# Kernel optimization log

Measured on AMD Instinct MI355X. Metric: run time of the kernel, lower is better.

## Reference

```python
import jax, jax.numpy as jnp
import numpy as np


def setup_inputs() -> dict:
    key = jax.random.key(0)
    ks = jax.random.split(key, 8)
    T, B, O, H, A = 512, 256, 720, 128, 2
    s = lambda k, shp, sc: (jax.random.normal(k, shp, jnp.float32) * sc)
    return {
        "x": jax.random.normal(ks[0], (T, B, O), jnp.float32),
        "h0": jnp.zeros((B, H), jnp.float32),
        "c0": jnp.zeros((B, H), jnp.float32),
        "Wx": s(ks[1], (O, 4 * H), 1.0 / np.sqrt(O)),
        "Wh": s(ks[2], (H, 4 * H), 1.0 / np.sqrt(H)),
        "b": jnp.zeros((4 * H,), jnp.float32),
        "Wa1": s(ks[3], (H, H), np.sqrt(2.0 / H)),
        "ba1": jnp.zeros((H,), jnp.float32),
        "Wa2": s(ks[4], (H, A), 0.01),
        "ba2": jnp.zeros((A,), jnp.float32),
        "log_std": jnp.zeros((A,), jnp.float32),
        "Wc1": s(ks[5], (H, H), np.sqrt(2.0 / H)),
        "bc1": jnp.zeros((H,), jnp.float32),
        "Wc2": s(ks[6], (H, 1), 0.01),
        "bc2": jnp.zeros((1,), jnp.float32),
    }


def _lstm(x, h0, c0, Wx, Wh, b):
    # Precompute input projections for all timesteps: [T, B, 4H]
    xW = jnp.einsum('tbo,og->tbg', x, Wx) + b

    def step(carry, xw_t):
        h, c = carry
        gates = xw_t + h @ Wh  # [B, 4H]
        i, f, g, o = jnp.split(gates, 4, axis=-1)
        c = jax.nn.sigmoid(f) * c + jax.nn.sigmoid(i) * jnp.tanh(g)
        h = jax.nn.sigmoid(o) * jnp.tanh(c)
        return (h, c), h

    (hT, cT), _ = jax.lax.scan(step, (h0, c0), xW)
    return hT, cT


def reference(x, h0, c0, Wx, Wh, b, Wa1, ba1, Wa2, ba2, log_std,
              Wc1, bc1, Wc2, bc2):
    hT, cT = _lstm(x, h0, c0, Wx, Wh, b)
    feat = hT  # outputs[-1] == last hidden state (unidirectional)
    actor_mean = jnp.tanh(feat @ Wa1 + ba1) @ Wa2 + ba2  # [B, A]
    std = jnp.exp(log_std)  # [A]
    value = (jnp.tanh(feat @ Wc1 + bc1) @ Wc2 + bc2).squeeze(-1)  # [B]
    return actor_mean, std, value, hT, cT
```

## Files before the change

kernel.cpp:

```cpp
#include <hip/hip_runtime.h>
#include <hip/hip_bf16.h>

typedef unsigned int   u32;
typedef unsigned short u16;
typedef _Float16       f16;
typedef __attribute__((ext_vector_type(2))) _Float16 f16x2;
typedef __attribute__((ext_vector_type(8))) _Float16 f16x8;
typedef __attribute__((ext_vector_type(4))) float    f32x4;
typedef __attribute__((ext_vector_type(4))) u32      u32x4;

#define T_STEPS 512
#define BATCH   256
#define O_IN    720
#define KPAD    736
#define HID     128
#define G4      512
#define OUT_STD 512
#define OUT_VAL 514
#define OUT_HT  770
#define OUT_CT  33538

static const unsigned long long XW_OFF  = 0ull;
static const unsigned long long WXT_OFF = 134217728ull;

__device__ inline float exp2raw(float x){
  float r; asm("v_exp_f32 %0, %1" : "=v"(r) : "v"(x)); return r;
}
__device__ inline float rcpraw(float x){
  float r; asm("v_rcp_f32 %0, %1" : "=v"(r) : "v"(x)); return r;
}
__device__ inline float tanhfast(float x){
  return fmaf(2.f, rcpraw(1.0f + exp2raw(-2.88539008f * x)), -1.f);
}

__device__ inline float dot2f(u32 a, u32 b, float c){
  float d;
  asm("v_dot2_f32_f16 %0, %1, %2, %3" : "=v"(d) : "v"(a), "v"(b), "v"(c));
  return d;
}

#define HH_STRIDE 144
#define H_BYTES   (2*HH_STRIDE)
#define HW_OFF(j) (((j)>>6)*HH_STRIDE + ((j)&63)*2)

__global__ void k_pack_wxt(const float* __restrict__ Wx, u16* __restrict__ wxt){
  const int n = blockIdx.x;
  for (int k = threadIdx.x; k < KPAD; k += 256){
    float v = (k < O_IN) ? Wx[(size_t)k * G4 + n] : 0.f;
    wxt[(size_t)n * KPAD + k] = __builtin_bit_cast(u16, (f16)v);
  }
}

__global__ __launch_bounds__(256, 2) void k_gemm(const float* __restrict__ x,
                                                 const u16* __restrict__ wxt,
                                                 u16* __restrict__ xw)
{
  const int l  = threadIdx.x & 63;
  const int w  = threadIdx.x >> 6;
  const int lr = l & 15;
  const int lk = l >> 4;
  const u32 L  = (blockIdx.x & 7u) * 256u + (blockIdx.x >> 3);
  const u32 mb = L >> 2, nb = L & 3u;
  const u32 M0 = mb * 256u + (u32)w * 64u;
  const u32 N0 = nb * 128u;

  const float* ax[4];
  const u16*   bx[8];
#pragma unroll
  for (int mf = 0; mf < 4; ++mf)
    ax[mf] = x + (unsigned long long)(M0 + mf*16 + lr) * O_IN + lk*8;
#pragma unroll
  for (int nf = 0; nf < 8; ++nf)
    bx[nf] = wxt + (unsigned long long)(N0 + nf*16 + lr) * KPAD + lk*8;

  f32x4 acc[4][8];
#pragma unroll
  for (int mf = 0; mf < 4; ++mf)
#pragma unroll
    for (int nf = 0; nf < 8; ++nf)
      acc[mf][nf] = (f32x4){0.f, 0.f, 0.f, 0.f};

  f32x4 a0[4][2];
  f16x8 aF[4], bF[8];

#pragma unroll
  for (int mf = 0; mf < 4; ++mf){
    a0[mf][0] = *(const f32x4*)(ax[mf]);
    a0[mf][1] = *(const f32x4*)(ax[mf] + 4);
  }
#pragma unroll
  for (int nf = 0; nf < 8; ++nf)
    bF[nf] = *(const f16x8*)(bx[nf]);
#pragma unroll
  for (int mf = 0; mf < 4; ++mf){
    f32x4 lo = a0[mf][0], hi = a0[mf][1];
    f16x8 v; v[0]=(f16)lo.x; v[1]=(f16)lo.y; v[2]=(f16)lo.z; v[3]=(f16)lo.w;
             v[4]=(f16)hi.x; v[5]=(f16)hi.y; v[6]=(f16)hi.z; v[7]=(f16)hi.w;
    aF[mf] = v;
  }

  for (int kc = 0; kc < 22; ++kc){
    if (kc < 21){
#pragma unroll
      for (int mf = 0; mf < 4; ++mf){
        a0[mf][0] = *(const f32x4*)(ax[mf] + (kc+1)*32);
        a0[mf][1] = *(const f32x4*)(ax[mf] + (kc+1)*32 + 4);
      }
    }
#pragma unroll
    for (int nf = 0; nf < 8; ++nf){
#pragma unroll
      for (int mf = 0; mf < 4; ++mf)
        acc[mf][nf] = __builtin_amdgcn_mfma_f32_16x16x32_f16(aF[mf], bF[nf], acc[mf][nf], 0, 0, 0);
      if (kc < 21)
        bF[nf] = *(const f16x8*)(bx[nf] + (kc+1)*32);
    }
    if (kc < 21){
#pragma unroll
      for (int mf = 0; mf < 4; ++mf){
        f32x4 lo = a0[mf][0], hi = a0[mf][1];
        f16x8 v; v[0]=(f16)lo.x; v[1]=(f16)lo.y; v[2]=(f16)lo.z; v[3]=(f16)lo.w;
                 v[4]=(f16)hi.x; v[5]=(f16)hi.y; v[6]=(f16)hi.z; v[7]=(f16)hi.w;
        aF[mf] = v;
      }
    }
  }

  {
    f16x8 aT[4];
#pragma unroll
    for (int mf = 0; mf < 4; ++mf) aT[mf] = (f16x8)(f16)0.f;
    if (lk < 2){
#pragma unroll
      for (int mf = 0; mf < 4; ++mf){
        f32x4 lo = *(const f32x4*)(ax[mf] + 704);
        f32x4 hi = *(const f32x4*)(ax[mf] + 708);
        f16x8 v; v[0]=(f16)lo.x; v[1]=(f16)lo.y; v[2]=(f16)lo.z; v[3]=(f16)lo.w;
                 v[4]=(f16)hi.x; v[5]=(f16)hi.y; v[6]=(f16)hi.z; v[7]=(f16)hi.w;
        aT[mf] = v;
      }
    }
#pragma unroll
    for (int nf = 0; nf < 8; ++nf){
      f16x8 bT = *(const f16x8*)(bx[nf] + 704);
#pragma unroll
      for (int mf = 0; mf < 4; ++mf)
        acc[mf][nf] = __builtin_amdgcn_mfma_f32_16x16x32_f16(aT[mf], bT, acc[mf][nf], 0, 0, 0);
    }
  }

#pragma unroll
  for (int mf = 0; mf < 4; ++mf){
    const u32 rowb = M0 + mf*16 + lk*4;
#pragma unroll
    for (int nf = 0; nf < 8; ++nf){
      const u32 col = N0 + nf*16 + lr;
#pragma unroll
      for (int r = 0; r < 4; ++r)
        xw[(unsigned long long)(rowb + r) * G4 + col] = __builtin_bit_cast(u16, (f16)acc[mf][nf][r]);
    }
  }
}

__global__ __attribute__((amdgpu_flat_work_group_size(1024,1024), amdgpu_waves_per_eu(4,4)))
void k_rnn(
    const u16* __restrict__ xw, const float* __restrict__ Wh,
    const float* __restrict__ h0, const float* __restrict__ c0,
    const float* __restrict__ bvec,
    const float* __restrict__ Wa1, const float* __restrict__ ba1,
    const float* __restrict__ Wa2, const float* __restrict__ ba2,
    const float* __restrict__ Wc1, const float* __restrict__ bc1,
    const float* __restrict__ Wc2, const float* __restrict__ bc2,
    const float* __restrict__ log_std, float* __restrict__ out)
{
  const int b = blockIdx.x;
  const int t = threadIdx.x;
  const int j = t >> 3;
  const int g = (t >> 1) & 3;
  const int q = t & 1;
  const int l = t & 63;
  const int lb = l & 56;

  __shared__ __align__(16) char hbuf[H_BYTES];
  __shared__ __align__(16) float hf[HID];
  __shared__ float hid[256];

  u32 wg[32];
#pragma unroll
  for (int m = 0; m < 32; ++m){
    const u32 kb = (u32)(64*q + 2*m) * G4 + (u32)(j + 128*g);
    f16x2 p; p[0] = (f16)Wh[kb]; p[1] = (f16)Wh[kb + G4];
    wg[m] = __builtin_bit_cast(u32, p);
  }
#pragma unroll
  for (int m = 0; m < 32; ++m) asm volatile("" : "+v"(wg[m]));

  const float bb = bvec[j + 128*g];
  const float kexp  = (g == 2) ? -2.88539008f : -1.44269504f;
  const float postm = (g == 2) ? 2.f : 1.f;
  const float posta = (g == 2) ? -1.f : 0.f;

  float cs = c0[b*HID + j];
  float hv = h0[b*HID + j];
  if ((t & 7) == 0)
    *(u16*)(hbuf + HW_OFF(j)) = __builtin_bit_cast(u16, (f16)hv);
  __syncthreads();

  const u16* xp = xw + (u32)b * G4 + (u32)(j + 128*g);
  float xc  = (float)__builtin_bit_cast(f16, xp[0]) + bb;
  float xn1 = (T_STEPS > 1) ? (float)__builtin_bit_cast(f16, xp[131072u]) + bb : 0.f;

  for (int s = 0; s < T_STEPS; ++s){
    const char* hq = hbuf + q * HH_STRIDE;

    float xn2 = 0.f;
    if (s + 2 < T_STEPS)
      xn2 = (float)__builtin_bit_cast(f16, xp[(u32)(s+2) * 131072u]) + bb;

    float p0 = 0.f, p1 = 0.f, p2 = 0.f, p3 = 0.f;
#pragma unroll
    for (int it = 0; it < 8; ++it){
      u32x4 hh = *(const u32x4*)(hq + it*16);
      p0 = dot2f(hh.x, wg[4*it+0], p0);
      p1 = dot2f(hh.y, wg[4*it+1], p1);
      p2 = dot2f(hh.z, wg[4*it+2], p2);
      p3 = dot2f(hh.w, wg[4*it+3], p3);
    }
    float p = (p0 + p1) + (p2 + p3);
    p += __shfl_xor(p, 1);

    float gval = p + xc;
    float av   = fmaf(postm, rcpraw(1.0f + exp2raw(kexp * gval)), posta);

    float ai = __shfl(av, lb | 0);
    float af = __shfl(av, lb | 2);
    float ag = __shfl(av, lb | 4);
    float ao = __shfl(av, lb | 6);

    cs = af * cs + ai * ag;
    hv = ao * tanhfast(cs);

    __syncthreads();
    if ((t & 7) == 0)
      *(u16*)(hbuf + HW_OFF(j)) = __builtin_bit_cast(u16, (f16)hv);
    __syncthreads();
    xc = xn1; xn1 = xn2;
  }

  if ((t & 7) == 0){
    out[OUT_HT + b*HID + j] = hv;
    out[OUT_CT + b*HID + j] = cs;
    hf[j] = hv;
  }
  __syncthreads();

  if (t < 256){
    const float* W = (t < HID) ? Wa1 : Wc1;
    const int col  = t & (HID - 1);
    const f32x4* hp4 = (const f32x4*)hf;
    float a0 = 0.f, a1 = 0.f, a2 = 0.f, a3 = 0.f;
#pragma unroll
    for (int qq = 0; qq < 32; ++qq){
      f32x4 hh = hp4[qq];
      a0 = fmaf(hh.x, W[(u32)(4*qq+0)*HID + col], a0);
      a1 = fmaf(hh.y, W[(u32)(4*qq+1)*HID + col], a1);
      a2 = fmaf(hh.z, W[(u32)(4*qq+2)*HID + col], a2);
      a3 = fmaf(hh.w, W[(u32)(4*qq+3)*HID + col], a3);
    }
    float a = (a0 + a1) + (a2 + a3);
    hid[t] = (t < HID) ? tanhfast(a + ba1[col]) : tanhfast(a + bc1[col]);
  }
  __syncthreads();

  {
    const int wv = t >> 6, lane = t & 63;
    float p = 0.f;
    if (wv == 0)      p = hid[lane]     * Wa2[lane*2]   + hid[lane+64]     * Wa2[(lane+64)*2];
    else if (wv == 1) p = hid[lane]     * Wa2[lane*2+1] + hid[lane+64]     * Wa2[(lane+64)*2+1];
    else if (wv == 2) p = hid[128+lane] * Wc2[lane]     + hid[128+lane+64] * Wc2[lane+64];
    if (wv < 3){
#pragma unroll
      for (int off = 32; off > 0; off >>= 1) p += __shfl_down(p, off);
      if (lane == 0){
        if (wv == 0) out[b*2 + 0]   = p + ba2[0];
        if (wv == 1) out[b*2 + 1]   = p + ba2[1];
        if (wv == 2) out[OUT_VAL+b] = p + bc2[0];
      }
    }
    if (b == 0 && wv == 3 && lane < 2) out[OUT_STD + lane] = expf(log_std[lane]);
  }
}

extern "C" void kernel_launch(void* const* d_in, const int* in_sizes, int n_in,
                              void* d_out, int out_size, void* d_ws, size_t ws_size,
                              hipStream_t stream)
{
  (void)in_sizes; (void)n_in; (void)out_size; (void)ws_size;
  const float* x    = (const float*)d_in[0];
  const float* h0   = (const float*)d_in[1];
  const float* c0   = (const float*)d_in[2];
  const float* Wx   = (const float*)d_in[3];
  const float* Wh   = (const float*)d_in[4];
  const float* bv   = (const float*)d_in[5];
  const float* Wa1  = (const float*)d_in[6];
  const float* ba1  = (const float*)d_in[7];
  const float* Wa2  = (const float*)d_in[8];
  const float* ba2  = (const float*)d_in[9];
  const float* lstd = (const float*)d_in[10];
  const float* Wc1  = (const float*)d_in[11];
  const float* bc1  = (const float*)d_in[12];
  const float* Wc2  = (const float*)d_in[13];
  const float* bc2  = (const float*)d_in[14];
  float* out = (float*)d_out;
  char*  ws  = (char*)d_ws;

  u16* xw  = (u16*)(ws + XW_OFF);
  u16* wxt = (u16*)(ws + WXT_OFF);

  k_pack_wxt<<<dim3(512),  dim3(256),  0, stream>>>(Wx, wxt);
  k_gemm<<<dim3(2048),     dim3(256),  0, stream>>>(x, wxt, xw);
  k_rnn<<<dim3(256),       dim3(1024), 0, stream>>>(xw, Wh, h0, c0, bv,
                                                    Wa1, ba1, Wa2, ba2, Wc1, bc1, Wc2, bc2,
                                                    lstd, out);
}
```

Measured before the change: 865.5 us.

## Split recurrent dot product over K across 8 lanes with DPP reduction

Reworks the per-step recurrent matvec in the LSTM kernel. Each of the 8 lanes per hidden unit now holds a 16-wide K slice of Wh for all four gates, instead of one gate over 64 K. Each lane does 32 dot2 ops over 2 LDS vector loads in place of 8. The partial sums are combined with a DPP transpose-reduce plus one shuffle, and gate broadcasts use DPP quad_perm instead of ds_bpermute shuffles. The aim is to cut LDS traffic and shuffle latency on the serial critical path, at the cost of extra select and DPP instructions.

Measured after the change: 815.4 us. -5.8%, faster.

```diff
diff --git a/kernel.cpp b/kernel.cpp
--- a/kernel.cpp
+++ b/kernel.cpp
@@ -39,9 +39,8 @@
   return d;
 }
 
-#define HH_STRIDE 144
-#define H_BYTES   (2*HH_STRIDE)
-#define HW_OFF(j) (((j)>>6)*HH_STRIDE + ((j)&63)*2)
+#define DPPF(x, ctrl) \
+  __uint_as_float((u32)__builtin_amdgcn_update_dpp(0, (int)__float_as_uint(x), (ctrl), 0xF, 0xF, false))
 
 __global__ void k_pack_wxt(const float* __restrict__ Wx, u16* __restrict__ wxt){
   const int n = blockIdx.x;
@@ -176,73 +175,94 @@
   const int b = blockIdx.x;
   const int t = threadIdx.x;
   const int j = t >> 3;
-  const int g = (t >> 1) & 3;
-  const int q = t & 1;
+  const int q = t & 7;
   const int l = t & 63;
-  const int lb = l & 56;
-
-  __shared__ __align__(16) char hbuf[H_BYTES];
+  const int gsel = l & 3;
+
+  __shared__ __align__(16) u16   hbuf[HID];
   __shared__ __align__(16) float hf[HID];
   __shared__ float hid[256];
 
-  u32 wg[32];
-#pragma unroll
-  for (int m = 0; m < 32; ++m){
-    const u32 kb = (u32)(64*q + 2*m) * G4 + (u32)(j + 128*g);
-    f16x2 p; p[0] = (f16)Wh[kb]; p[1] = (f16)Wh[kb + G4];
-    wg[m] = __builtin_bit_cast(u32, p);
-  }
-#pragma unroll
-  for (int m = 0; m < 32; ++m) asm volatile("" : "+v"(wg[m]));
-
-  const float bb = bvec[j + 128*g];
-  const float kexp  = (g == 2) ? -2.88539008f : -1.44269504f;
-  const float postm = (g == 2) ? 2.f : 1.f;
-  const float posta = (g == 2) ? -1.f : 0.f;
+  u32 wi[8], wf[8], wg[8], wo[8];
+#pragma unroll
+  for (int m = 0; m < 8; ++m){
+    const u32 kb = (u32)(16*q + 2*m) * G4 + (u32)j;
+    f16x2 p;
+    p[0]=(f16)Wh[kb      ]; p[1]=(f16)Wh[kb+G4      ]; wi[m]=__builtin_bit_cast(u32,p);
+    p[0]=(f16)Wh[kb+128  ]; p[1]=(f16)Wh[kb+G4+128  ]; wf[m]=__builtin_bit_cast(u32,p);
+    p[0]=(f16)Wh[kb+256  ]; p[1]=(f16)Wh[kb+G4+256  ]; wg[m]=__builtin_bit_cast(u32,p);
+    p[0]=(f16)Wh[kb+384  ]; p[1]=(f16)Wh[kb+G4+384  ]; wo[m]=__builtin_bit_cast(u32,p);
+  }
+#pragma unroll
+  for (int m = 0; m < 8; ++m){
+    asm volatile("" : "+v"(wi[m]));
+    asm volatile("" : "+v"(wf[m]));
+    asm volatile("" : "+v"(wg[m]));
+    asm volatile("" : "+v"(wo[m]));
+  }
+
+  const float bb = bvec[j + 128*gsel];
+  const float kexp  = (gsel == 2) ? -2.88539008f : -1.44269504f;
+  const float postm = (gsel == 2) ? 2.f : 1.f;
+  const float posta = (gsel == 2) ? -1.f : 0.f;
 
   float cs = c0[b*HID + j];
   float hv = h0[b*HID + j];
   if ((t & 7) == 0)
-    *(u16*)(hbuf + HW_OFF(j)) = __builtin_bit_cast(u16, (f16)hv);
+    hbuf[j] = __builtin_bit_cast(u16, (f16)hv);
   __syncthreads();
 
-  const u16* xp = xw + (u32)b * G4 + (u32)(j + 128*g);
+  const u16* xp = xw + (u32)b * G4 + (u32)(j + 128*gsel);
   float xc  = (float)__builtin_bit_cast(f16, xp[0]) + bb;
   float xn1 = (T_STEPS > 1) ? (float)__builtin_bit_cast(f16, xp[131072u]) + bb : 0.f;
 
   for (int s = 0; s < T_STEPS; ++s){
-    const char* hq = hbuf + q * HH_STRIDE;
+    const char* hq = (const char*)hbuf + 32*q;
+    u32x4 ha = *(const u32x4*)(hq);
+    u32x4 hb = *(const u32x4*)(hq + 16);
 
     float xn2 = 0.f;
     if (s + 2 < T_STEPS)
       xn2 = (float)__builtin_bit_cast(f16, xp[(u32)(s+2) * 131072u]) + bb;
 
-    float p0 = 0.f, p1 = 0.f, p2 = 0.f, p3 = 0.f;
-#pragma unroll
-    for (int it = 0; it < 8; ++it){
-      u32x4 hh = *(const u32x4*)(hq + it*16);
-      p0 = dot2f(hh.x, wg[4*it+0], p0);
-      p1 = dot2f(hh.y, wg[4*it+1], p1);
-      p2 = dot2f(hh.z, wg[4*it+2], p2);
-      p3 = dot2f(hh.w, wg[4*it+3], p3);
-    }
-    float p = (p0 + p1) + (p2 + p3);
-    p += __shfl_xor(p, 1);
-
-    float gval = p + xc;
+    float pi = 0.f, pf = 0.f, pg = 0.f, po = 0.f;
+#pragma unroll
+    for (int z = 0; z < 4; ++z){
+      pi = dot2f(ha[z], wi[z], pi);
+      pf = dot2f(ha[z], wf[z], pf);
+      pg = dot2f(ha[z], wg[z], pg);
+      po = dot2f(ha[z], wo[z], po);
+    }
+#pragma unroll
+    for (int z = 0; z < 4; ++z){
+      pi = dot2f(hb[z], wi[4+z], pi);
+      pf = dot2f(hb[z], wf[4+z], pf);
+      pg = dot2f(hb[z], wg[4+z], pg);
+      po = dot2f(hb[z], wo[4+z], po);
+    }
+
+    float k0 = (l & 1) ? pf : pi,  s0 = (l & 1) ? pi : pf;
+    float k1 = (l & 1) ? po : pg,  s1 = (l & 1) ? pg : po;
+    k0 += DPPF(s0, 177);
+    k1 += DPPF(s1, 177);
+    float k2 = (l & 2) ? k1 : k0,  s2 = (l & 2) ? k0 : k1;
+    k2 += DPPF(s2, 78);
+    k2 += __shfl_xor(k2, 4);
+
+    float gval = k2 + xc;
     float av   = fmaf(postm, rcpraw(1.0f + exp2raw(kexp * gval)), posta);
 
-    float ai = __shfl(av, lb | 0);
-    float af = __shfl(av, lb | 2);
-    float ag = __shfl(av, lb | 4);
-    float ao = __shfl(av, lb | 6);
+    float ai = DPPF(av, 0);
+    float af = DPPF(av, 85);
+    float ag = DPPF(av, 170);
+    float ao = DPPF(av, 255);
 
     cs = af * cs + ai * ag;
     hv = ao * tanhfast(cs);
 
     __syncthreads();
     if ((t & 7) == 0)
-      *(u16*)(hbuf + HW_OFF(j)) = __builtin_bit_cast(u16, (f16)hv);
+      hbuf[j] = __builtin_bit_cast(u16, (f16)hv);
     __syncthreads();
     xc = xn1; xn1 = xn2;
   }
```
